# Performance work log

Hardware: AMD Instinct MI355X
Metric: run time of the kernel (lower is better)

## Reference

```python
import jax, jax.numpy as jnp
import numpy as np

B, S, HID = 1, 2048, 2048
H = 16
DN, DR, DV = 128, 64, 128          # qk_nope_head_dim, qk_rope_head_dim, v_head_dim
DQ = DN + DR                        # q_head_dim = 192
QLR, KVLR = 1536, 512               # q_lora_rank, kv_lora_rank
MAXP = 32 * 1024
SCALE = DQ ** -0.5
EPS = 1e-6


def rmsnorm(x, w):
    return x * jax.lax.rsqrt(jnp.mean(x * x, axis=-1, keepdims=True) + EPS) * w


def rotate_half(x):
    h = x.shape[-1] // 2
    return jnp.concatenate((-x[..., h:], x[..., :h]), axis=-1)


def interleave_to_half(x):
    # torch: view(b,h,s,d//2,2).transpose(4,3).reshape(b,h,s,d)
    b, h, s, d = x.shape
    return x.reshape(b, h, s, d // 2, 2).transpose(0, 1, 2, 4, 3).reshape(b, h, s, d)


def setup_inputs() -> dict:
    key = jax.random.key(0)
    ks = jax.random.split(key, 8)
    def w(k, shape):
        fan_in = shape[-1]
        return jax.random.normal(k, shape, jnp.float32) * (fan_in ** -0.5)
    inp = {
        "hidden_states": jax.random.normal(ks[0], (B, S, HID), jnp.float32),
        "q_a_w": w(ks[1], (QLR, HID)),
        "q_a_ln": jnp.ones((QLR,), jnp.float32),
        "q_b_w": w(ks[2], (H * DQ, QLR)),
        "kv_a_w": w(ks[3], (KVLR + DR, HID)),
        "kv_a_ln": jnp.ones((KVLR,), jnp.float32),
        "kv_b_w": w(ks[4], (H * (DN + DV), KVLR)),
        "o_w": w(ks[5], (HID, H * DV)),
    }
    # rotary tables, seq_len = 32k
    inv_freq = 1.0 / (10000.0 ** (np.arange(0, DR, 2, dtype=np.float32) / DR))
    t = np.arange(MAXP, dtype=np.float32)
    freqs = np.outer(t, inv_freq)
    emb = np.concatenate((freqs, freqs), axis=-1)
    inp["cos"] = jnp.asarray(np.cos(emb), jnp.float32)
    inp["sin"] = jnp.asarray(np.sin(emb), jnp.float32)
    # bool mask, True = masked (causal)
    inp["attention_mask"] = jnp.triu(jnp.ones((S, S), bool), 1)[None, None]
    inp["position_ids"] = jnp.arange(S, dtype=jnp.int64 if jax.config.jax_enable_x64 else jnp.int32)[None].repeat(B, 0)
    return inp


def reference(hidden_states, q_a_w, q_a_ln, q_b_w, kv_a_w, kv_a_ln, kv_b_w, o_w,
              cos, sin, attention_mask, position_ids):
    b, s, _ = hidden_states.shape
    # low-rank Q: q_b(LN(q_a(x)))
    q = rmsnorm(hidden_states @ q_a_w.T, q_a_ln) @ q_b_w.T         # [b,s,H*DQ]
    q = q.reshape(b, s, H, DQ).transpose(0, 2, 1, 3)               # [b,H,s,DQ]
    q_nope, q_pe = q[..., :DN], q[..., DN:]
    # compressed KV + decoupled rope key
    ckv = hidden_states @ kv_a_w.T                                  # [b,s,KVLR+DR]
    compressed_kv, k_pe = ckv[..., :KVLR], ckv[..., KVLR:]
    k_pe = k_pe.reshape(b, s, 1, DR).transpose(0, 2, 1, 3)          # [b,1,s,DR]
    kv = rmsnorm(compressed_kv, kv_a_ln) @ kv_b_w.T                 # [b,s,H*(DN+DV)]
    kv = kv.reshape(b, s, H, DN + DV).transpose(0, 2, 1, 3)         # [b,H,s,DN+DV]
    k_nope, value_states = kv[..., :DN], kv[..., DN:]
    # rotary with interleaved->half reorder on the rope slice only
    cos_p = cos[position_ids][:, None]                              # [b,1,s,DR]
    sin_p = sin[position_ids][:, None]
    q_pe = interleave_to_half(q_pe)
    k_pe = interleave_to_half(k_pe)
    q_pe = q_pe * cos_p + rotate_half(q_pe) * sin_p
    k_pe = k_pe * cos_p + rotate_half(k_pe) * sin_p
    query_states = jnp.concatenate((q_nope, q_pe), axis=-1)         # [b,H,s,DQ]
    key_states = jnp.concatenate(
        (k_nope, jnp.broadcast_to(k_pe, (b, H, s, DR))), axis=-1)   # [b,H,s,DQ]
    # manual attention
    scores = jnp.einsum("bhqd,bhkd->bhqk", query_states, key_states) * SCALE
    scores = jnp.where(attention_mask, jnp.float32(-10000.0), scores)
    attn = jax.nn.softmax(scores.astype(jnp.float32), axis=-1).astype(query_states.dtype)
    attn_out = jnp.einsum("bhqk,bhkd->bhqd", attn, value_states)    # [b,H,s,DV]
    attn_out = attn_out.transpose(0, 2, 1, 3).reshape(b, s, H * DV)
    return attn_out @ o_w.T                                         # [b,s,HID]
```

## Files before the change

kernel.cpp:

```cpp
#include <hip/hip_runtime.h>
#include <stdint.h>

typedef unsigned short u16;
typedef __attribute__((ext_vector_type(8))) short short8;
typedef __attribute__((ext_vector_type(4))) float f32x4;
typedef __attribute__((ext_vector_type(4))) unsigned short ushort4_t;
typedef __attribute__((ext_vector_type(4))) float float4_t;

#define DEV_INLINE __device__ __forceinline__

DEV_INLINE u16 f2bf(float f) {
    union { float f; unsigned u; } x; x.f = f;
    unsigned u = x.u;
    unsigned r = (u + 0x7FFFu + ((u >> 16) & 1u)) >> 16;
    return (u16)r;
}

DEV_INLINE float bf2f(u16 b) {
    union { unsigned u; float f; } x; x.u = ((unsigned)b) << 16;
    return x.f;
}

DEV_INLINE float fexp2(float x) {
    float r;
    asm("v_exp_f32 %0, %1" : "=v"(r) : "v"(x));
    return r;
}

__global__ void conv_multi(const float* __restrict__ s0, u16* __restrict__ d0, long e0,
                           const float* __restrict__ s1, u16* __restrict__ d1, long e1,
                           const float* __restrict__ s2, u16* __restrict__ d2, long e2,
                           const float* __restrict__ s3, u16* __restrict__ d3, long e3,
                           const float* __restrict__ s4, u16* __restrict__ d4, long e4) {
    long i = (long)blockIdx.x * 256 + threadIdx.x;
    const float* s; u16* d; long base;
    if      (i < e0) { s = s0; d = d0; base = 0; }
    else if (i < e1) { s = s1; d = d1; base = e0; }
    else if (i < e2) { s = s2; d = d2; base = e1; }
    else if (i < e3) { s = s3; d = d3; base = e2; }
    else if (i < e4) { s = s4; d = d4; base = e3; }
    else return;
    long j = i - base;
    float4_t v = ((const float4_t*)s)[j];
    ushort4_t o;
    o.x = f2bf(v.x); o.y = f2bf(v.y); o.z = f2bf(v.z); o.w = f2bf(v.w);
    ((ushort4_t*)d)[j] = o;
}

__global__ void conv_pad(const float* __restrict__ in, u16* __restrict__ out,
                         int rows_valid, long n4, int cols4) {
    long i = (long)blockIdx.x * blockDim.x + threadIdx.x;
    if (i >= n4) return;
    long row = i / cols4;
    ushort4_t o; o.x = 0; o.y = 0; o.z = 0; o.w = 0;
    if (row < rows_valid) {
        float4_t v = ((const float4_t*)in)[i];
        o.x = f2bf(v.x); o.y = f2bf(v.y); o.z = f2bf(v.z); o.w = f2bf(v.w);
    }
    ((ushort4_t*)out)[i] = o;
}

#define BK 32

DEV_INLINE void gload16(const u16* g, u16* l) {
    __builtin_amdgcn_global_load_lds((const __attribute__((address_space(1))) unsigned int*)g,
                                     (__attribute__((address_space(3))) unsigned int*)l,
                                     16, 0, 0);
}

template <typename OT>
__global__ __launch_bounds__(256) void gemm64_db(const u16* __restrict__ A, const u16* __restrict__ B,
                                                 OT* __restrict__ C, int M, int N, int K) {
    __shared__ u16 As[2][64 * BK];
    __shared__ u16 Bs[2][128 * BK];
    const int tid = threadIdx.x;
    const int wid = tid >> 6, lane = tid & 63;
    const int lm = lane & 15, lk = lane >> 4;
    const long bm = (long)blockIdx.y * 64, bn = (long)blockIdx.x * 128;

    f32x4 acc[4][2] = {};

    const int rowS = lane >> 2;
    const int colS = ((lane & 3) ^ ((lane >> 3) & 3)) * 8;
    const int cs = (lm >> 1) & 3;
    const u16* Ag = A + (bm + wid * 16 + rowS) * (long)K + colS;
    const u16* Bg = B + (bn + wid * 32 + rowS) * (long)K + colS;
    const int aoff = wid * 16 * BK;
    const int boff = wid * 32 * BK;

    gload16(Ag, &As[0][aoff]);
    gload16(Bg, &Bs[0][boff]);
    gload16(Bg + 16 * (long)K, &Bs[0][boff + 16 * BK]);
    __syncthreads();

    int cur = 0;
    for (int k0 = 0; k0 < K; k0 += BK) {
        if (k0 + BK < K) {
            gload16(Ag + k0 + BK, &As[cur ^ 1][aoff]);
            gload16(Bg + k0 + BK, &Bs[cur ^ 1][boff]);
            gload16(Bg + 16 * (long)K + k0 + BK, &Bs[cur ^ 1][boff + 16 * BK]);
        }
        short8 af[4], bfr[2];
#pragma unroll
        for (int m = 0; m < 4; ++m)
            af[m] = *(const short8*)&As[cur][(m * 16 + lm) * BK + (lk ^ cs) * 8];
#pragma unroll
        for (int n = 0; n < 2; ++n)
            bfr[n] = *(const short8*)&Bs[cur][(wid * 32 + n * 16 + lm) * BK + (lk ^ cs) * 8];
#pragma unroll
        for (int m = 0; m < 4; ++m)
#pragma unroll
            for (int n = 0; n < 2; ++n)
                acc[m][n] = __builtin_amdgcn_mfma_f32_16x16x32_bf16(af[m], bfr[n], acc[m][n], 0, 0, 0);
        __syncthreads();
        cur ^= 1;
    }

#pragma unroll
    for (int m = 0; m < 4; ++m)
#pragma unroll
        for (int n = 0; n < 2; ++n)
#pragma unroll
            for (int r = 0; r < 4; ++r) {
                long idx = (bm + m * 16 + lk * 4 + r) * (long)N + bn + wid * 32 + n * 16 + lm;
                if constexpr (sizeof(OT) == 4) C[idx] = acc[m][n][r];
                else                           C[idx] = f2bf(acc[m][n][r]);
            }
}

__global__ __launch_bounds__(256) void rmsnorm_bf16(const float* __restrict__ in, const float* __restrict__ w,
                                                    u16* __restrict__ out, int ldin, int ldout, int ncols) {
    const int row = blockIdx.x, tid = threadIdx.x;
    const float* x = in + (long)row * ldin;
    float ss = 0.f;
    for (int c = tid; c < ncols; c += 256) { float v = x[c]; ss = fmaf(v, v, ss); }
#pragma unroll
    for (int off = 32; off > 0; off >>= 1) ss += __shfl_down(ss, off);
    __shared__ float part[4];
    if ((tid & 63) == 0) part[tid >> 6] = ss;
    __syncthreads();
    float tot = part[0] + part[1] + part[2] + part[3];
    float rs = rsqrtf(tot / (float)ncols + 1e-6f);
    for (int c = tid; c < ncols; c += 256) out[(long)row * ldout + c] = f2bf(x[c] * rs * w[c]);
}

__global__ void rope_k(const float* __restrict__ ckv, const int* __restrict__ pos,
                       const float* __restrict__ cosT, const float* __restrict__ sinT,
                       u16* __restrict__ Kb) {
    int idx = blockIdx.x * 256 + threadIdx.x;
    if (idx >= 2048 * 32) return;
    int s = idx >> 5, j = idx & 31;
    long p = pos[s];
    const float* row = ckv + (long)s * 2176 + 2048;
    float x0 = row[2 * j], x1 = row[2 * j + 1];
    float c0 = cosT[p * 64 + j],      s0 = sinT[p * 64 + j];
    float c1 = cosT[p * 64 + 32 + j], s1 = sinT[p * 64 + 32 + j];
    u16 o0 = f2bf(x0 * c0 - x1 * s0);
    u16 o1 = f2bf(x1 * c1 + x0 * s1);
#pragma unroll
    for (int h = 0; h < 16; ++h) {
        u16* kr = Kb + ((long)h * 2048 + s) * 192 + 128;
        kr[j] = o0; kr[32 + j] = o1;
    }
}

__global__ void build_q(const u16* __restrict__ q, const int* __restrict__ pos,
                        const float* __restrict__ cosT, const float* __restrict__ sinT,
                        u16* __restrict__ Qb) {
    long idx = (long)blockIdx.x * 256 + threadIdx.x;
    if (idx >= 16L * 2048 * 192) return;
    int d = (int)(idx % 192);
    int s = (int)((idx / 192) % 2048);
    int h = (int)(idx / (192L * 2048));
    const u16* qrow = q + (long)s * 3072 + h * 192;
    u16 outv;
    if (d < 128) {
        outv = qrow[d];
    } else {
        long p = pos[s];
        int dd = d - 128;
        float cv = cosT[p * 64 + dd], sv = sinT[p * 64 + dd];
        float val;
        if (dd < 32) val = bf2f(qrow[128 + 2 * dd]) * cv - bf2f(qrow[128 + 2 * dd + 1]) * sv;
        else { int jj = dd - 32; val = bf2f(qrow[128 + 2 * jj + 1]) * cv + bf2f(qrow[128 + 2 * jj]) * sv; }
        outv = f2bf(val);
    }
    Qb[((long)h * 2048 + s) * 192 + d] = outv;
}

__global__ __launch_bounds__(256) void build_kv2(const u16* __restrict__ kv, u16* __restrict__ Kb,
                                                 u16* __restrict__ Vt) {
    __shared__ u16 Ls[128][72];
    const int h = blockIdx.y, s0 = blockIdx.x * 64;
    const int tid = threadIdx.x;
#pragma unroll
    for (int i = 0; i < 8; ++i) {
        int u = i * 256 + tid;
        int r = u >> 5, c8 = (u & 31) * 8;
        short8 x = *(const short8*)(kv + (long)(s0 + r) * 4096 + h * 256 + c8);
        if (c8 < 128) {
            *(short8*)(Kb + ((long)h * 2048 + s0 + r) * 192 + c8) = x;
        } else {
#pragma unroll
            for (int j = 0; j < 8; ++j) {
                int d = c8 - 128 + j;
                Ls[d][r ^ (((d >> 3) & 7) << 3)] = (u16)x[j];
            }
        }
    }
    __syncthreads();
#pragma unroll
    for (int i = 0; i < 8; ++i) {
        int u = i * 256 + tid;
        int d = u >> 4, s4 = (u & 15) * 4;
        int swz = ((d >> 3) & 7) << 3;
        ushort4_t v;
        v.x = Ls[d][(s4 + 0) ^ swz]; v.y = Ls[d][(s4 + 1) ^ swz];
        v.z = Ls[d][(s4 + 2) ^ swz]; v.w = Ls[d][(s4 + 3) ^ swz];
        *(ushort4_t*)(Vt + ((long)h * 128 + d) * 2048 + s0 + s4) = v;
    }
}

__global__ __launch_bounds__(512, 2) void attn_fwd(const u16* __restrict__ Qb, const u16* __restrict__ Kb,
                                                   const u16* __restrict__ Vt, u16* __restrict__ Ao) {
    __shared__ __align__(16) char smem[52736];

    const int b = blockIdx.x;
    const int h = (b & 7) * 2 + ((b >> 3) & 1);
    const int pi = b >> 4;
    const int tid = threadIdx.x;
    const int wid = tid >> 6, lane = tid & 63;
    const int lm = lane & 15, lk = lane >> 4;
    const int s = wid >> 2;
    const int wp = wid & 3;
    const int t256 = tid & 255;

    u16* KsS = (u16*)(smem) + s * 6400;
    u16* VsS = (u16*)(smem + 25600) + s * 4096;
    u16* PsW = (u16*)(smem + 41984) + wid * 640;
    float* ML = (float*)(smem + 52224);
    float* Ob = (float*)smem;

    const u16* Kh = Kb + (long)h * 2048 * 192;
    const u16* Vh = Vt + (long)h * 128 * 2048;

    short8 bones = {};
    if (lm == 0) {
#pragma unroll
        for (int j = 0; j < 8; ++j) bones[j] = (short)0x3F80;
    }
    const float C2 = 0.104117548f;

    for (int half = 0; half < 2; ++half) {
        const int qi = half ? (31 - pi) : pi;
        const int q0 = qi * 64;
        const int nt = 2 * qi + 2;
        const int niter = qi + 1;

        short8 qf[6];
        const u16* qbase = Qb + ((long)h * 2048 + q0 + wp * 16 + lm) * 192;
#pragma unroll
        for (int kf = 0; kf < 6; ++kf) qf[kf] = *(const short8*)(qbase + kf * 32 + lk * 8);

        f32x4 o[8] = {};
        f32x4 o9 = {};
        float mrow[4] = {-1e30f, -1e30f, -1e30f, -1e30f};

        short8 kreg[3], vreg[2];
        {
            const long k0 = s * 32;
#pragma unroll
            for (int i = 0; i < 3; ++i) {
                int idx = i * 256 + t256; int r = idx / 24, c = (idx % 24) * 8;
                kreg[i] = *(const short8*)(Kh + (k0 + r) * 192 + c);
            }
#pragma unroll
            for (int i = 0; i < 2; ++i) {
                int idx = i * 256 + t256; int dv = idx >> 2, kvb = idx & 3;
                vreg[i] = *(const short8*)(Vh + (long)dv * 2048 + k0 + kvb * 8);
            }
#pragma unroll
            for (int i = 0; i < 3; ++i) {
                int idx = i * 256 + t256; int r = idx / 24, c = (idx % 24) * 8;
                *(short8*)&KsS[r * 200 + c] = kreg[i];
            }
#pragma unroll
            for (int i = 0; i < 2; ++i) {
                int idx = i * 256 + t256; int dv = idx >> 2, kvb = idx & 3;
                *(short8*)&VsS[kvb * 1024 + ((dv * 8) ^ (kvb * 16))] = vreg[i];
            }
        }
        __syncthreads();

        for (int it = 0; it < niter; ++it) {
            const int ts = 2 * it + s;
            const int k0 = ts * 32;
            const bool more = (it + 1 < niter);

            if (more) {
                const long k0n = (long)(2 * (it + 1) + s) * 32;
#pragma unroll
                for (int i = 0; i < 3; ++i) {
                    int idx = i * 256 + t256; int r = idx / 24, c = (idx % 24) * 8;
                    kreg[i] = *(const short8*)(Kh + (k0n + r) * 192 + c);
                }
#pragma unroll
                for (int i = 0; i < 2; ++i) {
                    int idx = i * 256 + t256; int dv = idx >> 2, kvb = idx & 3;
                    vreg[i] = *(const short8*)(Vh + (long)dv * 2048 + k0n + kvb * 8);
                }
            }

            f32x4 sfr[2] = {};
            __builtin_amdgcn_s_setprio(1);
#pragma unroll
            for (int n = 0; n < 2; ++n)
#pragma unroll
                for (int kf = 0; kf < 6; ++kf) {
                    short8 kb = *(const short8*)&KsS[(n * 16 + lm) * 200 + kf * 32 + lk * 8];
                    sfr[n] = __builtin_amdgcn_mfma_f32_16x16x32_bf16(qf[kf], kb, sfr[n], 0, 0, 0);
                }
            __builtin_amdgcn_s_setprio(0);

            float sv[2][4];
            const bool bt = (ts >= nt - 2);
#pragma unroll
            for (int n = 0; n < 2; ++n)
#pragma unroll
                for (int r = 0; r < 4; ++r) {
                    float val = sfr[n][r] * C2;
                    if (bt && (k0 + n * 16 + lm > q0 + wp * 16 + lk * 4 + r)) val = -1e30f;
                    sv[n][r] = val;
                }

            float pmax[4];
#pragma unroll
            for (int r = 0; r < 4; ++r) {
                float mx = fmaxf(sv[0][r], sv[1][r]);
#pragma unroll
                for (int off = 1; off < 16; off <<= 1) mx = fmaxf(mx, __shfl_xor(mx, off));
                pmax[r] = mx;
            }
            bool need = (pmax[0] > mrow[0] + 8.f) || (pmax[1] > mrow[1] + 8.f) ||
                        (pmax[2] > mrow[2] + 8.f) || (pmax[3] > mrow[3] + 8.f);
            if (__any(need)) {
#pragma unroll
                for (int r = 0; r < 4; ++r) {
                    float mnew = fmaxf(mrow[r], pmax[r]);
                    float alpha = fexp2(mrow[r] - mnew);
                    mrow[r] = mnew;
#pragma unroll
                    for (int d = 0; d < 8; ++d) o[d][r] *= alpha;
                    o9[r] *= alpha;
                }
            }
#pragma unroll
            for (int n = 0; n < 2; ++n)
#pragma unroll
                for (int r = 0; r < 4; ++r)
                    PsW[(lk * 4 + r) * 40 + ((n * 16 + lm) ^ (lk << 3))] = f2bf(fexp2(sv[n][r] - mrow[r]));

            short8 pf = *(const short8*)&PsW[lm * 40 + ((lk ^ ((lm >> 2) & 3)) << 3)];
            __builtin_amdgcn_s_setprio(1);
#pragma unroll
            for (int d = 0; d < 8; ++d) {
                short8 vf = *(const short8*)&VsS[lk * 1024 + (((d * 16 + lm) * 8) ^ (lk * 16))];
                o[d] = __builtin_amdgcn_mfma_f32_16x16x32_bf16(pf, vf, o[d], 0, 0, 0);
            }
            o9 = __builtin_amdgcn_mfma_f32_16x16x32_bf16(pf, bones, o9, 0, 0, 0);
            __builtin_amdgcn_s_setprio(0);

            if (more) {
                __syncthreads();
#pragma unroll
                for (int i = 0; i < 3; ++i) {
                    int idx = i * 256 + t256; int r = idx / 24, c = (idx % 24) * 8;
                    *(short8*)&KsS[r * 200 + c] = kreg[i];
                }
#pragma unroll
                for (int i = 0; i < 2; ++i) {
                    int idx = i * 256 + t256; int dv = idx >> 2, kvb = idx & 3;
                    *(short8*)&VsS[kvb * 1024 + ((dv * 8) ^ (kvb * 16))] = vreg[i];
                }
                __syncthreads();
            }
        }

        __syncthreads();
        if (s == 1) {
#pragma unroll
            for (int d = 0; d < 8; ++d)
#pragma unroll
                for (int r = 0; r < 4; ++r)
                    Ob[(wp * 16 + lk * 4 + r) * 128 + d * 16 + lm] = o[d][r];
            if (lm == 0) {
#pragma unroll
                for (int r = 0; r < 4; ++r) {
                    ML[(wp * 16 + lk * 4 + r) * 2 + 0] = mrow[r];
                    ML[(wp * 16 + lk * 4 + r) * 2 + 1] = o9[r];
                }
            }
        }
        __syncthreads();
        if (s == 0) {
            float e0[4], e1[4], inv[4];
#pragma unroll
            for (int r = 0; r < 4; ++r) {
                float m1 = ML[(wp * 16 + lk * 4 + r) * 2 + 0];
                float l1 = ML[(wp * 16 + lk * 4 + r) * 2 + 1];
                float l0 = __shfl(o9[r], lane & 48);
                float M = fmaxf(mrow[r], m1);
                e0[r] = fexp2(mrow[r] - M);
                e1[r] = fexp2(m1 - M);
                inv[r] = 1.f / (l0 * e0[r] + l1 * e1[r]);
            }
#pragma unroll
            for (int d = 0; d < 8; ++d)
#pragma unroll
                for (int r = 0; r < 4; ++r) {
                    float val = (o[d][r] * e0[r] +
                                 Ob[(wp * 16 + lk * 4 + r) * 128 + d * 16 + lm] * e1[r]) * inv[r];
                    Ao[((long)q0 + wp * 16 + lk * 4 + r) * 2048 + h * 128 + d * 16 + lm] = f2bf(val);
                }
        }
        __syncthreads();
    }
}

extern "C" void kernel_launch(void* const* d_in, const int* in_sizes, int n_in,
                              void* d_out, int out_size, void* d_ws, size_t ws_size,
                              hipStream_t stream) {
    (void)in_sizes; (void)n_in; (void)out_size; (void)ws_size;
    const float* hidden  = (const float*)d_in[0];
    const float* q_a_w   = (const float*)d_in[1];
    const float* q_a_ln  = (const float*)d_in[2];
    const float* q_b_w   = (const float*)d_in[3];
    const float* kv_a_w  = (const float*)d_in[4];
    const float* kv_a_ln = (const float*)d_in[5];
    const float* kv_b_w  = (const float*)d_in[6];
    const float* o_w     = (const float*)d_in[7];
    const float* cosT    = (const float*)d_in[8];
    const float* sinT    = (const float*)d_in[9];
    const int*   pos     = (const int*)d_in[11];

    char* ws = (char*)d_ws;
    u16* o_w_bf   = (u16*)(ws + 0);
    u16* qb_w_bf  = (u16*)(ws + 8388608);
    u16* kvb_w_bf = (u16*)(ws + 17825792);
    u16* qn_bf    = (u16*)(ws + 22020096);
    u16* kvn_bf   = (u16*)(ws + 28311552);
    u16* Qb       = (u16*)(ws + 30408704);
    u16* Kb       = (u16*)(ws + 42991616);
    u16* Vt       = (u16*)(ws + 55574528);
    u16* aout_bf  = (u16*)(ws + 63963136);
    u16*   hid_bf    = (u16*)(ws + 72351744);
    u16*   qkva_w_bf = (u16*)(ws + 80740352);
    float* qkva_f    = (float*)(ws + 89653248);
    u16*   q_f_bf    = (u16*)(ws + 72351744);
    u16*   kv_f_bf   = (u16*)(ws + 89653248);

    conv_multi<<<17920, 256, 0, stream>>>(
        hidden, hid_bf,               1048576L,
        q_a_w,  qkva_w_bf,            1835008L,
        q_b_w,  qb_w_bf,              3014656L,
        kv_b_w, kvb_w_bf,             3538944L,
        o_w,    o_w_bf,               4587520L);
    conv_pad<<<(640L*2048/4 + 255)/256, 256, 0, stream>>>(kv_a_w, qkva_w_bf + 1536L*2048, 576, 640L*2048/4, 512);

    gemm64_db<float><<<dim3(17, 32), 256, 0, stream>>>(hid_bf, qkva_w_bf, qkva_f, 2048, 2176, 2048);

    rmsnorm_bf16<<<2048, 256, 0, stream>>>(qkva_f, q_a_ln, qn_bf, 2176, 1536, 1536);
    rmsnorm_bf16<<<2048, 256, 0, stream>>>(qkva_f + 1536, kv_a_ln, kvn_bf, 2176, 512, 512);
    rope_k<<<(2048*32)/256, 256, 0, stream>>>(qkva_f, pos, cosT, sinT, Kb);

    gemm64_db<u16><<<dim3(24, 32), 256, 0, stream>>>(qn_bf, qb_w_bf, q_f_bf, 2048, 3072, 1536);
    gemm64_db<u16><<<dim3(32, 32), 256, 0, stream>>>(kvn_bf, kvb_w_bf, kv_f_bf, 2048, 4096, 512);

    build_q<<<(unsigned)((16L*2048*192 + 255)/256), 256, 0, stream>>>(q_f_bf, pos, cosT, sinT, Qb);
    build_kv2<<<dim3(32, 16), 256, 0, stream>>>(kv_f_bf, Kb, Vt);

    attn_fwd<<<256, 512, 0, stream>>>(Qb, Kb, Vt, aout_bf);

    gemm64_db<float><<<dim3(16, 32), 256, 0, stream>>>(aout_bf, o_w_bf, (float*)d_out, 2048, 2048, 2048);
}
```

Before: 255.8 us.

## Use 128x128 GEMM tiles with split-K atomics and 128-row attention blocks

Replaces the 64x128 GEMM with a 128x128 tile kernel in which each wave computes a 64x64 sub-tile, raising MFMA-to-load reuse. The two fp32-output GEMMs gain split-K=2, accumulated with atomic adds into a buffer zeroed by a memset, so more blocks run. Attention now gives each block one 128-row query tile, with each wave handling two 16-row groups that share every K and V fragment load. This replaces the old pairing of a light and a heavy 64-row tile per block, so causal load balancing across blocks is lost, and the atomics make summation order nondeterministic.

```diff
diff --git a/kernel.cpp b/kernel.cpp
--- a/kernel.cpp
+++ b/kernel.cpp
@@ -68,49 +68,54 @@
                                      16, 0, 0);
 }
 
-template <typename OT>
-__global__ __launch_bounds__(256) void gemm64_db(const u16* __restrict__ A, const u16* __restrict__ B,
-                                                 OT* __restrict__ C, int M, int N, int K) {
-    __shared__ u16 As[2][64 * BK];
+template <typename OT, int SPLITK>
+__global__ __launch_bounds__(256) void gemm128_db(const u16* __restrict__ A, const u16* __restrict__ B,
+                                                  OT* __restrict__ C, int M, int N, int K) {
+    __shared__ u16 As[2][128 * BK];
     __shared__ u16 Bs[2][128 * BK];
     const int tid = threadIdx.x;
     const int wid = tid >> 6, lane = tid & 63;
     const int lm = lane & 15, lk = lane >> 4;
-    const long bm = (long)blockIdx.y * 64, bn = (long)blockIdx.x * 128;
-
-    f32x4 acc[4][2] = {};
+    const int wr = wid >> 1, wc = wid & 1;
+    const long bm = (long)blockIdx.y * 128, bn = (long)blockIdx.x * 128;
+    const int Kh = K / SPLITK;
+    const long kbase = (long)blockIdx.z * Kh;
+
+    f32x4 acc[4][4] = {};
 
     const int rowS = lane >> 2;
     const int colS = ((lane & 3) ^ ((lane >> 3) & 3)) * 8;
     const int cs = (lm >> 1) & 3;
-    const u16* Ag = A + (bm + wid * 16 + rowS) * (long)K + colS;
-    const u16* Bg = B + (bn + wid * 32 + rowS) * (long)K + colS;
-    const int aoff = wid * 16 * BK;
-    const int boff = wid * 32 * BK;
-
-    gload16(Ag, &As[0][aoff]);
-    gload16(Bg, &Bs[0][boff]);
-    gload16(Bg + 16 * (long)K, &Bs[0][boff + 16 * BK]);
+    const u16* Ag = A + (bm + wid * 16 + rowS) * (long)K + kbase + colS;
+    const u16* Bg = B + (bn + wid * 16 + rowS) * (long)K + kbase + colS;
+    const int off0 = wid * 512;
+    const int off1 = off0 + 64 * 32;
+
+    gload16(Ag, &As[0][off0]);
+    gload16(Ag + 64 * (long)K, &As[0][off1]);
+    gload16(Bg, &Bs[0][off0]);
+    gload16(Bg + 64 * (long)K, &Bs[0][off1]);
     __syncthreads();
 
     int cur = 0;
-    for (int k0 = 0; k0 < K; k0 += BK) {
-        if (k0 + BK < K) {
-            gload16(Ag + k0 + BK, &As[cur ^ 1][aoff]);
-            gload16(Bg + k0 + BK, &Bs[cur ^ 1][boff]);
-            gload16(Bg + 16 * (long)K + k0 + BK, &Bs[cur ^ 1][boff + 16 * BK]);
-        }
-        short8 af[4], bfr[2];
+    for (int k0 = 0; k0 < Kh; k0 += BK) {
+        if (k0 + BK < Kh) {
+            gload16(Ag + k0 + BK, &As[cur ^ 1][off0]);
+            gload16(Ag + 64 * (long)K + k0 + BK, &As[cur ^ 1][off1]);
+            gload16(Bg + k0 + BK, &Bs[cur ^ 1][off0]);
+            gload16(Bg + 64 * (long)K + k0 + BK, &Bs[cur ^ 1][off1]);
+        }
+        short8 af[4], bfr[4];
 #pragma unroll
         for (int m = 0; m < 4; ++m)
-            af[m] = *(const short8*)&As[cur][(m * 16 + lm) * BK + (lk ^ cs) * 8];
-#pragma unroll
-        for (int n = 0; n < 2; ++n)
-            bfr[n] = *(const short8*)&Bs[cur][(wid * 32 + n * 16 + lm) * BK + (lk ^ cs) * 8];
+            af[m] = *(const short8*)&As[cur][(wr * 64 + m * 16 + lm) * BK + (lk ^ cs) * 8];
+#pragma unroll
+        for (int n = 0; n < 4; ++n)
+            bfr[n] = *(const short8*)&Bs[cur][(wc * 64 + n * 16 + lm) * BK + (lk ^ cs) * 8];
 #pragma unroll
         for (int m = 0; m < 4; ++m)
 #pragma unroll
-            for (int n = 0; n < 2; ++n)
+            for (int n = 0; n < 4; ++n)
                 acc[m][n] = __builtin_amdgcn_mfma_f32_16x16x32_bf16(af[m], bfr[n], acc[m][n], 0, 0, 0);
         __syncthreads();
         cur ^= 1;
@@ -119,12 +124,17 @@
 #pragma unroll
     for (int m = 0; m < 4; ++m)
 #pragma unroll
-        for (int n = 0; n < 2; ++n)
+        for (int n = 0; n < 4; ++n)
 #pragma unroll
             for (int r = 0; r < 4; ++r) {
-                long idx = (bm + m * 16 + lk * 4 + r) * (long)N + bn + wid * 32 + n * 16 + lm;
-                if constexpr (sizeof(OT) == 4) C[idx] = acc[m][n][r];
-                else                           C[idx] = f2bf(acc[m][n][r]);
+                long idx = (bm + wr * 64 + m * 16 + lk * 4 + r) * (long)N + bn + wc * 64 + n * 16 + lm;
+                if constexpr (SPLITK > 1) {
+                    unsafeAtomicAdd((float*)&C[idx], acc[m][n][r]);
+                } else if constexpr (sizeof(OT) == 4) {
+                    C[idx] = acc[m][n][r];
+                } else {
+                    C[idx] = f2bf(acc[m][n][r]);
+                }
             }
 }
 
@@ -223,26 +233,26 @@
 
 __global__ __launch_bounds__(512, 2) void attn_fwd(const u16* __restrict__ Qb, const u16* __restrict__ Kb,
                                                    const u16* __restrict__ Vt, u16* __restrict__ Ao) {
-    __shared__ __align__(16) char smem[52736];
+    __shared__ __align__(16) char smem[63488];
 
     const int b = blockIdx.x;
-    const int h = (b & 7) * 2 + ((b >> 3) & 1);
-    const int pi = b >> 4;
+    const int h = b & 15, qi = b >> 4;
     const int tid = threadIdx.x;
     const int wid = tid >> 6, lane = tid & 63;
     const int lm = lane & 15, lk = lane >> 4;
-    const int s = wid >> 2;
-    const int wp = wid & 3;
+    const int s = wid >> 2, wp = wid & 3;
     const int t256 = tid & 255;
 
-    u16* KsS = (u16*)(smem) + s * 6400;
+    u16* KsS = (u16*)smem + s * 6400;
     u16* VsS = (u16*)(smem + 25600) + s * 4096;
-    u16* PsW = (u16*)(smem + 41984) + wid * 640;
-    float* ML = (float*)(smem + 52224);
+    u16* PsW = (u16*)(smem + 41984) + wid * 1280;
+    float* ML = (float*)(smem + 62464);
     float* Ob = (float*)smem;
 
     const u16* Kh = Kb + (long)h * 2048 * 192;
     const u16* Vh = Vt + (long)h * 128 * 2048;
+    const int q0 = qi * 128;
+    const int niter = 2 * (qi + 1);
 
     short8 bones = {};
     if (lm == 0) {
@@ -251,34 +261,140 @@
     }
     const float C2 = 0.104117548f;
 
-    for (int half = 0; half < 2; ++half) {
-        const int qi = half ? (31 - pi) : pi;
-        const int q0 = qi * 64;
-        const int nt = 2 * qi + 2;
-        const int niter = qi + 1;
-
-        short8 qf[6];
-        const u16* qbase = Qb + ((long)h * 2048 + q0 + wp * 16 + lm) * 192;
-#pragma unroll
-        for (int kf = 0; kf < 6; ++kf) qf[kf] = *(const short8*)(qbase + kf * 32 + lk * 8);
-
-        f32x4 o[8] = {};
-        f32x4 o9 = {};
-        float mrow[4] = {-1e30f, -1e30f, -1e30f, -1e30f};
-
-        short8 kreg[3], vreg[2];
-        {
-            const long k0 = s * 32;
+    short8 qf[2][6];
+#pragma unroll
+    for (int mg = 0; mg < 2; ++mg) {
+        const u16* qbase = Qb + ((long)h * 2048 + q0 + wp * 32 + mg * 16 + lm) * 192;
+#pragma unroll
+        for (int kf = 0; kf < 6; ++kf) qf[mg][kf] = *(const short8*)(qbase + kf * 32 + lk * 8);
+    }
+
+    f32x4 o[2][8] = {};
+    f32x4 o9[2] = {};
+    float mrow[2][4] = {{-1e30f, -1e30f, -1e30f, -1e30f}, {-1e30f, -1e30f, -1e30f, -1e30f}};
+
+    short8 kreg[3], vreg[2];
+    {
+        const long k0 = s * 32;
+#pragma unroll
+        for (int i = 0; i < 3; ++i) {
+            int idx = i * 256 + t256; int r = idx / 24, c = (idx % 24) * 8;
+            kreg[i] = *(const short8*)(Kh + (k0 + r) * 192 + c);
+        }
+#pragma unroll
+        for (int i = 0; i < 2; ++i) {
+            int idx = i * 256 + t256; int dv = idx >> 2, kvb = idx & 3;
+            vreg[i] = *(const short8*)(Vh + (long)dv * 2048 + k0 + kvb * 8);
+        }
+#pragma unroll
+        for (int i = 0; i < 3; ++i) {
+            int idx = i * 256 + t256; int r = idx / 24, c = (idx % 24) * 8;
+            *(short8*)&KsS[r * 200 + c] = kreg[i];
+        }
+#pragma unroll
+        for (int i = 0; i < 2; ++i) {
+            int idx = i * 256 + t256; int dv = idx >> 2, kvb = idx & 3;
+            *(short8*)&VsS[kvb * 1024 + ((dv * 8) ^ (kvb * 16))] = vreg[i];
+        }
+    }
+    __syncthreads();
+
+    for (int it = 0; it < niter; ++it) {
+        const int ts = 2 * it + s;
+        const int k0 = ts * 32;
+        const bool more = (it + 1 < niter);
+
+        if (more) {
+            const long k0n = (long)(ts + 2) * 32;
 #pragma unroll
             for (int i = 0; i < 3; ++i) {
                 int idx = i * 256 + t256; int r = idx / 24, c = (idx % 24) * 8;
-                kreg[i] = *(const short8*)(Kh + (k0 + r) * 192 + c);
+                kreg[i] = *(const short8*)(Kh + (k0n + r) * 192 + c);
             }
 #pragma unroll
             for (int i = 0; i < 2; ++i) {
                 int idx = i * 256 + t256; int dv = idx >> 2, kvb = idx & 3;
-                vreg[i] = *(const short8*)(Vh + (long)dv * 2048 + k0 + kvb * 8);
-            }
+                vreg[i] = *(const short8*)(Vh + (long)dv * 2048 + k0n + kvb * 8);
+            }
+        }
+
+        f32x4 sfr[2][2] = {};
+        __builtin_amdgcn_s_setprio(1);
+#pragma unroll
+        for (int kf = 0; kf < 6; ++kf)
+#pragma unroll
+            for (int n = 0; n < 2; ++n) {
+                short8 kb = *(const short8*)&KsS[(n * 16 + lm) * 200 + kf * 32 + lk * 8];
+#pragma unroll
+                for (int mg = 0; mg < 2; ++mg)
+                    sfr[mg][n] = __builtin_amdgcn_mfma_f32_16x16x32_bf16(qf[mg][kf], kb, sfr[mg][n], 0, 0, 0);
+            }
+        __builtin_amdgcn_s_setprio(0);
+
+        float sv[2][2][4];
+        const bool bt = (ts >= 4 * qi);
+#pragma unroll
+        for (int mg = 0; mg < 2; ++mg)
+#pragma unroll
+            for (int n = 0; n < 2; ++n)
+#pragma unroll
+                for (int r = 0; r < 4; ++r) {
+                    float val = sfr[mg][n][r] * C2;
+                    if (bt && (k0 + n * 16 + lm > q0 + wp * 32 + mg * 16 + lk * 4 + r)) val = -1e30f;
+                    sv[mg][n][r] = val;
+                }
+
+        float pmax[2][4];
+#pragma unroll
+        for (int mg = 0; mg < 2; ++mg)
+#pragma unroll
+            for (int r = 0; r < 4; ++r) {
+                float mx = fmaxf(sv[mg][0][r], sv[mg][1][r]);
+#pragma unroll
+                for (int off = 1; off < 16; off <<= 1) mx = fmaxf(mx, __shfl_xor(mx, off));
+                pmax[mg][r] = mx;
+            }
+        bool need = false;
+#pragma unroll
+        for (int mg = 0; mg < 2; ++mg)
+#pragma unroll
+            for (int r = 0; r < 4; ++r) need = need || (pmax[mg][r] > mrow[mg][r] + 8.f);
+        if (__any(need)) {
+#pragma unroll
+            for (int mg = 0; mg < 2; ++mg)
+#pragma unroll
+                for (int r = 0; r < 4; ++r) {
+                    float mnew = fmaxf(mrow[mg][r], pmax[mg][r]);
+                    float alpha = fexp2(mrow[mg][r] - mnew);
+                    mrow[mg][r] = mnew;
+#pragma unroll
+                    for (int d = 0; d < 8; ++d) o[mg][d][r] *= alpha;
+                    o9[mg][r] *= alpha;
+                }
+        }
+#pragma unroll
+        for (int mg = 0; mg < 2; ++mg)
+#pragma unroll
+            for (int n = 0; n < 2; ++n)
+#pragma unroll
+                for (int r = 0; r < 4; ++r)
+                    PsW[(mg * 16 + lk * 4 + r) * 40 + n * 16 + lm] = f2bf(fexp2(sv[mg][n][r] - mrow[mg][r]));
+
+        short8 pf0 = *(const short8*)&PsW[lm * 40 + lk * 8];
+        short8 pf1 = *(const short8*)&PsW[(16 + lm) * 40 + lk * 8];
+        __builtin_amdgcn_s_setprio(1);
+#pragma unroll
+        for (int d = 0; d < 8; ++d) {
+            short8 vf = *(const short8*)&VsS[lk * 1024 + (((d * 16 + lm) * 8) ^ (lk * 16))];
+            o[0][d] = __builtin_amdgcn_mfma_f32_16x16x32_bf16(pf0, vf, o[0][d], 0, 0, 0);
+            o[1][d] = __builtin_amdgcn_mfma_f32_16x16x32_bf16(pf1, vf, o[1][d], 0, 0, 0);
+        }
+        o9[0] = __builtin_amdgcn_mfma_f32_16x16x32_bf16(pf0, bones, o9[0], 0, 0, 0);
+        o9[1] = __builtin_amdgcn_mfma_f32_16x16x32_bf16(pf1, bones, o9[1], 0, 0, 0);
+        __builtin_amdgcn_s_setprio(0);
+
+        if (more) {
+            __syncthreads();
 #pragma unroll
             for (int i = 0; i < 3; ++i) {
                 int idx = i * 256 + t256; int r = idx / 24, c = (idx % 24) * 8;
@@ -289,139 +405,61 @@
                 int idx = i * 256 + t256; int dv = idx >> 2, kvb = idx & 3;
                 *(short8*)&VsS[kvb * 1024 + ((dv * 8) ^ (kvb * 16))] = vreg[i];
             }
-        }
-        __syncthreads();
-
-        for (int it = 0; it < niter; ++it) {
-            const int ts = 2 * it + s;
-            const int k0 = ts * 32;
-            const bool more = (it + 1 < niter);
-
-            if (more) {
-                const long k0n = (long)(2 * (it + 1) + s) * 32;
-#pragma unroll
-                for (int i = 0; i < 3; ++i) {
-                    int idx = i * 256 + t256; int r = idx / 24, c = (idx % 24) * 8;
-                    kreg[i] = *(const short8*)(Kh + (k0n + r) * 192 + c);
-                }
-#pragma unroll
-                for (int i = 0; i < 2; ++i) {
-                    int idx = i * 256 + t256; int dv = idx >> 2, kvb = idx & 3;
-                    vreg[i] = *(const short8*)(Vh + (long)dv * 2048 + k0n + kvb * 8);
-                }
-            }
-
-            f32x4 sfr[2] = {};
-            __builtin_amdgcn_s_setprio(1);
-#pragma unroll
-            for (int n = 0; n < 2; ++n)
-#pragma unroll
-                for (int kf = 0; kf < 6; ++kf) {
-                    short8 kb = *(const short8*)&KsS[(n * 16 + lm) * 200 + kf * 32 + lk * 8];
-                    sfr[n] = __builtin_amdgcn_mfma_f32_16x16x32_bf16(qf[kf], kb, sfr[n], 0, 0, 0);
-                }
-            __builtin_amdgcn_s_setprio(0);
-
-            float sv[2][4];
-            const bool bt = (ts >= nt - 2);
-#pragma unroll
-            for (int n = 0; n < 2; ++n)
-#pragma unroll
-                for (int r = 0; r < 4; ++r) {
-                    float val = sfr[n][r] * C2;
-                    if (bt && (k0 + n * 16 + lm > q0 + wp * 16 + lk * 4 + r)) val = -1e30f;
-                    sv[n][r] = val;
-                }
-
-            float pmax[4];
-#pragma unroll
-            for (int r = 0; r < 4; ++r) {
-                float mx = fmaxf(sv[0][r], sv[1][r]);
-#pragma unroll
-                for (int off = 1; off < 16; off <<= 1) mx = fmaxf(mx, __shfl_xor(mx, off));
-                pmax[r] = mx;
-            }
-            bool need = (pmax[0] > mrow[0] + 8.f) || (pmax[1] > mrow[1] + 8.f) ||
-                        (pmax[2] > mrow[2] + 8.f) || (pmax[3] > mrow[3] + 8.f);
-            if (__any(need)) {
-#pragma unroll
-                for (int r = 0; r < 4; ++r) {
-                    float mnew = fmaxf(mrow[r], pmax[r]);
-                    float alpha = fexp2(mrow[r] - mnew);
-                    mrow[r] = mnew;
-#pragma unroll
-                    for (int d = 0; d < 8; ++d) o[d][r] *= alpha;
-                    o9[r] *= alpha;
-                }
-            }
-#pragma unroll
-            for (int n = 0; n < 2; ++n)
-#pragma unroll
-                for (int r = 0; r < 4; ++r)
-                    PsW[(lk * 4 + r) * 40 + ((n * 16 + lm) ^ (lk << 3))] = f2bf(fexp2(sv[n][r] - mrow[r]));
-
-            short8 pf = *(const short8*)&PsW[lm * 40 + ((lk ^ ((lm >> 2) & 3)) << 3)];
-            __builtin_amdgcn_s_setprio(1);
-#pragma unroll
-            for (int d = 0; d < 8; ++d) {
-                short8 vf = *(const short8*)&VsS[lk * 1024 + (((d * 16 + lm) * 8) ^ (lk * 16))];
-                o[d] = __builtin_amdgcn_mfma_f32_16x16x32_bf16(pf, vf, o[d], 0, 0, 0);
-            }
-            o9 = __builtin_amdgcn_mfma_f32_16x16x32_bf16(pf, bones, o9, 0, 0, 0);
-            __builtin_amdgcn_s_setprio(0);
-
-            if (more) {
-                __syncthreads();
-#pragma unroll
-                for (int i = 0; i < 3; ++i) {
-                    int idx = i * 256 + t256; int r = idx / 24, c = (idx % 24) * 8;
-                    *(short8*)&KsS[r * 200 + c] = kreg[i];
-                }
-#pragma unroll
-                for (int i = 0; i < 2; ++i) {
-                    int idx = i * 256 + t256; int dv = idx >> 2, kvb = idx & 3;
-                    *(short8*)&VsS[kvb * 1024 + ((dv * 8) ^ (kvb * 16))] = vreg[i];
-                }
-                __syncthreads();
-            }
-        }
-
-        __syncthreads();
+            __syncthreads();
+        }
+    }
+
+    __syncthreads();
+    float e0[2][4], e1[2][4], invl[2][4];
+#pragma unroll
+    for (int p = 0; p < 2; ++p) {
         if (s == 1) {
 #pragma unroll
-            for (int d = 0; d < 8; ++d)
-#pragma unroll
-                for (int r = 0; r < 4; ++r)
-                    Ob[(wp * 16 + lk * 4 + r) * 128 + d * 16 + lm] = o[d][r];
-            if (lm == 0) {
-#pragma unroll
-                for (int r = 0; r < 4; ++r) {
-                    ML[(wp * 16 + lk * 4 + r) * 2 + 0] = mrow[r];
-                    ML[(wp * 16 + lk * 4 + r) * 2 + 1] = o9[r];
-                }
+            for (int mg = 0; mg < 2; ++mg)
+#pragma unroll
+                for (int dd = 0; dd < 4; ++dd)
+#pragma unroll
+                    for (int r = 0; r < 4; ++r)
+                        Ob[(wp * 32 + mg * 16 + lk * 4 + r) * 64 + dd * 16 + lm] = o[mg][p * 4 + dd][r];
+            if (p == 0 && lm == 0) {
+#pragma unroll
+                for (int mg = 0; mg < 2; ++mg)
+#pragma unroll
+                    for (int r = 0; r < 4; ++r) {
+                        int row = wp * 32 + mg * 16 + lk * 4 + r;
+                        ML[row * 2 + 0] = mrow[mg][r];
+                        ML[row * 2 + 1] = o9[mg][r];
+                    }
             }
         }
         __syncthreads();
         if (s == 0) {
-            float e0[4], e1[4], inv[4];
-#pragma unroll
-            for (int r = 0; r < 4; ++r) {
-                float m1 = ML[(wp * 16 + lk * 4 + r) * 2 + 0];
-                float l1 = ML[(wp * 16 + lk * 4 + r) * 2 + 1];
-                float l0 = __shfl(o9[r], lane & 48);
-                float M = fmaxf(mrow[r], m1);
-                e0[r] = fexp2(mrow[r] - M);
-                e1[r] = fexp2(m1 - M);
-                inv[r] = 1.f / (l0 * e0[r] + l1 * e1[r]);
-            }
-#pragma unroll
-            for (int d = 0; d < 8; ++d)
-#pragma unroll
-                for (int r = 0; r < 4; ++r) {
-                    float val = (o[d][r] * e0[r] +
-                                 Ob[(wp * 16 + lk * 4 + r) * 128 + d * 16 + lm] * e1[r]) * inv[r];
-                    Ao[((long)q0 + wp * 16 + lk * 4 + r) * 2048 + h * 128 + d * 16 + lm] = f2bf(val);
-                }
+            if (p == 0) {
+#pragma unroll
+                for (int mg = 0; mg < 2; ++mg)
+#pragma unroll
+                    for (int r = 0; r < 4; ++r) {
+                        int row = wp * 32 + mg * 16 + lk * 4 + r;
+                        float m1 = ML[row * 2 + 0];
+                        float l1 = ML[row * 2 + 1];
+                        float l0 = __shfl(o9[mg][r], lane & 48);
+                        float M = fmaxf(mrow[mg][r], m1);
+                        e0[mg][r] = fexp2(mrow[mg][r] - M);
+                        e1[mg][r] = fexp2(m1 - M);
+                        invl[mg][r] = 1.f / (l0 * e0[mg][r] + l1 * e1[mg][r]);
+                    }
+            }
+#pragma unroll
+            for (int mg = 0; mg < 2; ++mg)
+#pragma unroll
+                for (int dd = 0; dd < 4; ++dd)
+#pragma unroll
+                    for (int r = 0; r < 4; ++r) {
+                        int row = wp * 32 + mg * 16 + lk * 4 + r;
+                        float val = (o[mg][p * 4 + dd][r] * e0[mg][r] +
+                                     Ob[row * 64 + dd * 16 + lm] * e1[mg][r]) * invl[mg][r];
+                        Ao[((long)q0 + row) * 2048 + h * 128 + (p * 4 + dd) * 16 + lm] = f2bf(val);
+                    }
         }
         __syncthreads();
     }
@@ -460,26 +498,28 @@
     u16*   kv_f_bf   = (u16*)(ws + 89653248);
 
     conv_multi<<<17920, 256, 0, stream>>>(
-        hidden, hid_bf,               1048576L,
-        q_a_w,  qkva_w_bf,            1835008L,
-        q_b_w,  qb_w_bf,              3014656L,
-        kv_b_w, kvb_w_bf,             3538944L,
-        o_w,    o_w_bf,               4587520L);
+        hidden, hid_bf,    1048576L,
+        q_a_w,  qkva_w_bf, 1835008L,
+        q_b_w,  qb_w_bf,   3014656L,
+        kv_b_w, kvb_w_bf,  3538944L,
+        o_w,    o_w_bf,    4587520L);
     conv_pad<<<(640L*2048/4 + 255)/256, 256, 0, stream>>>(kv_a_w, qkva_w_bf + 1536L*2048, 576, 640L*2048/4, 512);
 
-    gemm64_db<float><<<dim3(17, 32), 256, 0, stream>>>(hid_bf, qkva_w_bf, qkva_f, 2048, 2176, 2048);
+    hipMemsetAsync(qkva_f, 0, 2048L * 2176 * 4, stream);
+    gemm128_db<float, 2><<<dim3(17, 16, 2), 256, 0, stream>>>(hid_bf, qkva_w_bf, qkva_f, 2048, 2176, 2048);
 
     rmsnorm_bf16<<<2048, 256, 0, stream>>>(qkva_f, q_a_ln, qn_bf, 2176, 1536, 1536);
     rmsnorm_bf16<<<2048, 256, 0, stream>>>(qkva_f + 1536, kv_a_ln, kvn_bf, 2176, 512, 512);
     rope_k<<<(2048*32)/256, 256, 0, stream>>>(qkva_f, pos, cosT, sinT, Kb);
 
-    gemm64_db<u16><<<dim3(24, 32), 256, 0, stream>>>(qn_bf, qb_w_bf, q_f_bf, 2048, 3072, 1536);
-    gemm64_db<u16><<<dim3(32, 32), 256, 0, stream>>>(kvn_bf, kvb_w_bf, kv_f_bf, 2048, 4096, 512);
+    gemm128_db<u16, 1><<<dim3(24, 16), 256, 0, stream>>>(qn_bf, qb_w_bf, q_f_bf, 2048, 3072, 1536);
+    gemm128_db<u16, 1><<<dim3(32, 16), 256, 0, stream>>>(kvn_bf, kvb_w_bf, kv_f_bf, 2048, 4096, 512);
 
     build_q<<<(unsigned)((16L*2048*192 + 255)/256), 256, 0, stream>>>(q_f_bf, pos, cosT, sinT, Qb);
     build_kv2<<<dim3(32, 16), 256, 0, stream>>>(kv_f_bf, Kb, Vt);
 
     attn_fwd<<<256, 512, 0, stream>>>(Qb, Kb, Vt, aout_bf);
 
-    gemm64_db<float><<<dim3(16, 32), 256, 0, stream>>>(aout_bf, o_w_bf, (float*)d_out, 2048, 2048, 2048);
-}
+    hipMemsetAsync(d_out, 0, 2048L * 2048 * 4, stream);
+    gemm128_db<float, 2><<<dim3(16, 16, 2), 256, 0, stream>>>(aout_bf, o_w_bf, (float*)d_out, 2048, 2048, 2048);
+}
```

Measured after the change: 307.8 us (median of 3 runs). 1.2x slower.
